# Optimization experiments

Measured on AMD Instinct MI355X. Metric: run time of the kernel, lower is better.

## Reference

```python
import jax, jax.numpy as jnp
import numpy as np

NEG_INF = -1e9  # mask fill value used by the original layer
LEAKY_SLOPE = 0.2


def setup_inputs() -> dict:
    key = jax.random.key(0)
    k1, k2, k3, k4 = jax.random.split(key, 4)
    B, N, D_in = 8, 1024, 256
    H, head_dim = 8, 32  # output_dim=256, concat_heads=True
    node_features = jax.random.normal(k1, (B, N, D_in), dtype=jnp.float32)
    adjacency = jax.random.randint(k2, (B, N, N), 0, 2, dtype=jnp.int32)
    W = jax.random.normal(k3, (H, D_in, head_dim), dtype=jnp.float32) * (1.0 / np.sqrt(D_in))
    a = jax.random.normal(k4, (H, 2 * head_dim), dtype=jnp.float32) * (1.0 / np.sqrt(2 * head_dim))
    bias = jnp.zeros((H * head_dim,), dtype=jnp.float32)
    return {"node_features": node_features, "adjacency": adjacency, "W": W, "a": a, "bias": bias}


def reference(node_features, adjacency, W, a, bias):
    # node_features: (B,N,D_in); adjacency: (B,N,N) in {0,1}
    H, _, hd = W.shape
    # Per-head linear transform: (B,H,N,head_dim)
    Wh = jnp.einsum('bni,hij->bhnj', node_features, W)
    # a @ concat(h_i, h_j) == a1 @ h_i + a2 @ h_j  (avoids O(N^2*2hd) concat)
    a1, a2 = a[:, :hd], a[:, hd:]
    e_i = jnp.einsum('bhnj,hj->bhn', Wh, a1)  # (B,H,N) source term
    e_j = jnp.einsum('bhnj,hj->bhn', Wh, a2)  # (B,H,N) target term
    scores = e_i[:, :, :, None] + e_j[:, :, None, :]  # (B,H,N,N)
    # LeakyReLU(0.2) exactly as ops.maximum(x, 0.2*x)
    scores = jnp.maximum(scores, LEAKY_SLOPE * scores)
    mask = adjacency.astype(scores.dtype)[:, None, :, :]  # (B,1,N,N)
    masked = scores * mask + (1.0 - mask) * NEG_INF
    attn = jax.nn.softmax(masked, axis=-1)  # (B,H,N,N)
    attended = jnp.einsum('bhij,bhjk->bhik', attn, Wh)  # (B,H,N,hd)
    B, _, N, _ = attended.shape
    # concat heads -> (B,N,H*hd); head order matches the python loop concat
    out = attended.transpose(0, 2, 1, 3).reshape(B, N, H * hd)
    out = out + bias
    return jax.nn.relu(out)
```

## Files before the change

kernel.cpp:

```cpp
#include <hip/hip_runtime.h>

#define GAT_B   8
#define GAT_N   1024
#define GAT_DIN 256
#define GAT_H   8
#define GAT_HD  32

typedef unsigned short gu16;
typedef unsigned int   gu32;
typedef __bf16 bf16x8 __attribute__((ext_vector_type(8)));
typedef __bf16 bf16x4 __attribute__((ext_vector_type(4)));
typedef float  f32x4v __attribute__((ext_vector_type(4)));

__device__ __forceinline__ float gb2f(gu16 u) { return __uint_as_float(((gu32)u) << 16); }

__device__ __forceinline__ int gat_is_fp32(const gu16* p) {
    int bad = 0;
    for (int i = 0; i < 128; ++i) {
        int e = (p[i] >> 7) & 0xFF;
        if (e >= 140) bad = 1;
    }
    return bad;
}

__global__ __launch_bounds__(256) void CustomGATLayer_90348932038855_kernel(
    const void* __restrict__ Xv, const void* __restrict__ Wv, const void* __restrict__ Av,
    __bf16* __restrict__ whb, float* __restrict__ e1, float* __restrict__ e2)
{
    __shared__ __align__(16) __bf16 WlF[GAT_DIN * GAT_HD];
    __shared__ int sflag;

    const int t  = threadIdx.x;
    const int id = blockIdx.x;
    const int h  = id & 7;
    const int mg = id >> 3;

    if (t == 0) sflag = gat_is_fp32((const gu16*)Xv);
    __syncthreads();
    const int fp32 = sflag;

    if (fp32) {
        const float* ws = (const float*)Wv + (size_t)h * GAT_DIN * GAT_HD;
        #pragma unroll
        for (int q = 0; q < 8; ++q) {
            int idx = q * 1024 + t * 4;
            int i = idx >> 5, k = idx & 31;
            float4 v = *(const float4*)(ws + idx);
            int d = (((i >> 5) * 4 + ((i >> 3) & 3)) * 32 + k) * 8 + (i & 7);
            WlF[d] = (__bf16)v.x; WlF[d + 8]  = (__bf16)v.y;
            WlF[d + 16] = (__bf16)v.z; WlF[d + 24] = (__bf16)v.w;
        }
    } else {
        const gu16* ws = (const gu16*)Wv + (size_t)h * GAT_DIN * GAT_HD;
        gu16* wl = (gu16*)WlF;
        #pragma unroll
        for (int q = 0; q < 8; ++q) {
            int idx = q * 1024 + t * 4;
            int i = idx >> 5, k = idx & 31;
            ushort4 v = *(const ushort4*)(ws + idx);
            int d = (((i >> 5) * 4 + ((i >> 3) & 3)) * 32 + k) * 8 + (i & 7);
            wl[d] = v.x; wl[d + 8] = v.y; wl[d + 16] = v.z; wl[d + 24] = v.w;
        }
    }
    __syncthreads();

    const int wid = t >> 6, l = t & 63, g = l >> 4, c = l & 15;
    const int mt   = mg * 4 + wid;
    const int M0   = mt * 16;
    const int b    = M0 >> 10;
    const int nloc = M0 & 1023;
    const int row  = nloc + c;

    f32x4v acc0 = {0.f, 0.f, 0.f, 0.f};
    f32x4v acc1 = {0.f, 0.f, 0.f, 0.f};

    if (fp32) {
        const float* xb = (const float*)Xv + ((size_t)b * GAT_N + row) * GAT_DIN;
        #pragma unroll
        for (int kc = 0; kc < 8; ++kc) {
            float4 x0 = *(const float4*)(xb + kc * 32 + 8 * g);
            float4 x1 = *(const float4*)(xb + kc * 32 + 8 * g + 4);
            bf16x8 af;
            af[0] = (__bf16)x0.x; af[1] = (__bf16)x0.y; af[2] = (__bf16)x0.z; af[3] = (__bf16)x0.w;
            af[4] = (__bf16)x1.x; af[5] = (__bf16)x1.y; af[6] = (__bf16)x1.z; af[7] = (__bf16)x1.w;
            bf16x8 b0 = *(const bf16x8*)&WlF[((kc * 4 + g) * 32 + c) * 8];
            bf16x8 b1 = *(const bf16x8*)&WlF[((kc * 4 + g) * 32 + c + 16) * 8];
            acc0 = __builtin_amdgcn_mfma_f32_16x16x32_bf16(af, b0, acc0, 0, 0, 0);
            acc1 = __builtin_amdgcn_mfma_f32_16x16x32_bf16(af, b1, acc1, 0, 0, 0);
        }
    } else {
        const gu16* xb = (const gu16*)Xv + ((size_t)b * GAT_N + row) * GAT_DIN;
        #pragma unroll
        for (int kc = 0; kc < 8; ++kc) {
            bf16x8 af = *(const bf16x8*)(xb + kc * 32 + 8 * g);
            bf16x8 b0 = *(const bf16x8*)&WlF[((kc * 4 + g) * 32 + c) * 8];
            bf16x8 b1 = *(const bf16x8*)&WlF[((kc * 4 + g) * 32 + c + 16) * 8];
            acc0 = __builtin_amdgcn_mfma_f32_16x16x32_bf16(af, b0, acc0, 0, 0, 0);
            acc1 = __builtin_amdgcn_mfma_f32_16x16x32_bf16(af, b1, acc1, 0, 0, 0);
        }
    }

    const int nb = nloc + 4 * g;
    const int jc = nb >> 5, kg = (nb >> 3) & 3, e0 = nb & 7;
    const size_t fb = (((size_t)(b * GAT_H + h) * 32 + jc) * 4 + kg) * 32;
    bf16x4 v0, v1;
    v0[0] = (__bf16)acc0[0]; v0[1] = (__bf16)acc0[1];
    v0[2] = (__bf16)acc0[2]; v0[3] = (__bf16)acc0[3];
    v1[0] = (__bf16)acc1[0]; v1[1] = (__bf16)acc1[1];
    v1[2] = (__bf16)acc1[2]; v1[3] = (__bf16)acc1[3];
    *(bf16x4*)(whb + (fb + c) * 8 + e0)      = v0;
    *(bf16x4*)(whb + (fb + c + 16) * 8 + e0) = v1;

    float a1c, a1c16, a2c, a2c16;
    if (fp32) {
        const float* ap = (const float*)Av + h * 2 * GAT_HD;
        a1c = ap[c]; a1c16 = ap[c + 16]; a2c = ap[32 + c]; a2c16 = ap[48 + c];
    } else {
        const gu16* ap = (const gu16*)Av + h * 2 * GAT_HD;
        a1c = gb2f(ap[c]); a1c16 = gb2f(ap[c + 16]);
        a2c = gb2f(ap[32 + c]); a2c16 = gb2f(ap[48 + c]);
    }
    float p1[4], p2[4];
    #pragma unroll
    for (int q = 0; q < 4; ++q) {
        p1[q] = acc0[q] * a1c + acc1[q] * a1c16;
        p2[q] = acc0[q] * a2c + acc1[q] * a2c16;
        #pragma unroll
        for (int mm = 1; mm <= 8; mm <<= 1) {
            p1[q] += __shfl_xor(p1[q], mm);
            p2[q] += __shfl_xor(p2[q], mm);
        }
    }
    if (c == 0) {
        const size_t eb = (size_t)(b * GAT_H + h) * GAT_N + nb;
        #pragma unroll
        for (int q = 0; q < 4; ++q) { e1[eb + q] = p1[q]; e2[eb + q] = p2[q]; }
    }
}

__global__ __launch_bounds__(512) void CustomGATLayer_90348932038855_attn(
    const void* __restrict__ Xv, const int* __restrict__ adj, const void* __restrict__ biasv,
    const __bf16* __restrict__ whb, const float* __restrict__ e1f, const float* __restrict__ e2f,
    float* __restrict__ out)
{
    __shared__ __align__(16) float e2l[GAT_H * GAT_N];
    __shared__ int sflag;

    const int t = threadIdx.x;
    const int h = t >> 6, l = t & 63, g = l >> 4, c = l & 15;
    const int id = blockIdx.x;
    const int b = id & 7, tile = id >> 3;
    const int i0 = tile * 16;

    if (t == 0) sflag = gat_is_fp32((const gu16*)Xv);

    {
        const float* s = e2f + (size_t)(b * GAT_H + h) * GAT_N;
        float* d = e2l + h * GAT_N;
        #pragma unroll
        for (int q = 0; q < 4; ++q) {
            int off = (q * 64 + l) * 4;
            *(float4*)(d + off) = *(const float4*)(s + off);
        }
    }
    __syncthreads();
    const int fp32 = sflag;

    const float e1r = e1f[(size_t)(b * GAT_H + h) * GAT_N + i0 + c];
    const int* adjr = adj + ((size_t)(b * GAT_N + i0 + c)) * GAT_N + 8 * g;
    const __bf16* whr = whb + (size_t)(b * GAT_H + h) * (GAT_N * GAT_HD) + g * 256 + c * 8;
    const float* e2h = e2l + h * GAT_N + 8 * g;

    int4 pa0 = *(const int4*)(adjr);
    int4 pa1 = *(const int4*)(adjr + 4);
    bf16x8 pw0 = *(const bf16x8*)(whr);
    bf16x8 pw1 = *(const bf16x8*)(whr + 128);

    f32x4v acc0 = {0.f, 0.f, 0.f, 0.f};
    f32x4v acc1 = {0.f, 0.f, 0.f, 0.f};
    float dsum = 0.f;

#define GAT_WCOMP(EV, AV, IDX) {                    \
        float s_ = e1r + (EV);                      \
        s_ = fmaxf(s_, 0.2f * s_);                  \
        s_ = fminf(s_, 60.0f);                      \
        float w_ = __expf(s_);                      \
        w_ = (AV) ? w_ : 0.0f;                      \
        dsum += w_;                                 \
        pf[IDX] = (__bf16)w_; }

    #pragma unroll 4
    for (int jc = 0; jc < 32; ++jc) {
        int4 a0 = pa0, a1 = pa1;
        bf16x8 w0 = pw0, w1 = pw1;
        if (jc < 31) {
            const int* an = adjr + (jc + 1) * 32;
            pa0 = *(const int4*)(an);
            pa1 = *(const int4*)(an + 4);
            const __bf16* wn = whr + (jc + 1) * 1024;
            pw0 = *(const bf16x8*)(wn);
            pw1 = *(const bf16x8*)(wn + 128);
        }
        float4 ea = *(const float4*)(e2h + jc * 32);
        float4 eb = *(const float4*)(e2h + jc * 32 + 4);
        bf16x8 pf;
        GAT_WCOMP(ea.x, a0.x, 0) GAT_WCOMP(ea.y, a0.y, 1)
        GAT_WCOMP(ea.z, a0.z, 2) GAT_WCOMP(ea.w, a0.w, 3)
        GAT_WCOMP(eb.x, a1.x, 4) GAT_WCOMP(eb.y, a1.y, 5)
        GAT_WCOMP(eb.z, a1.z, 6) GAT_WCOMP(eb.w, a1.w, 7)
        acc0 = __builtin_amdgcn_mfma_f32_16x16x32_bf16(pf, w0, acc0, 0, 0, 0);
        acc1 = __builtin_amdgcn_mfma_f32_16x16x32_bf16(pf, w1, acc1, 0, 0, 0);
    }
#undef GAT_WCOMP

    dsum += __shfl_xor(dsum, 16);
    dsum += __shfl_xor(dsum, 32);

    float bv0, bv1;
    if (fp32) {
        const float* bp = (const float*)biasv + h * GAT_HD;
        bv0 = bp[c]; bv1 = bp[c + 16];
    } else {
        const gu16* bp = (const gu16*)biasv + h * GAT_HD;
        bv0 = gb2f(bp[c]); bv1 = gb2f(bp[c + 16]);
    }

    float* ob = out + (size_t)(b * GAT_N + i0) * (GAT_H * GAT_HD) + h * GAT_HD + c;
    #pragma unroll
    for (int q = 0; q < 4; ++q) {
        float d = __shfl(dsum, 4 * g + q);
        float r = (d > 0.f) ? (1.0f / d) : 0.0f;
        float o0 = acc0[q] * r + bv0;
        float o1 = acc1[q] * r + bv1;
        o0 = fmaxf(o0, 0.f); o1 = fmaxf(o1, 0.f);
        ob[(size_t)(4 * g + q) * (GAT_H * GAT_HD)]      = o0;
        ob[(size_t)(4 * g + q) * (GAT_H * GAT_HD) + 16] = o1;
    }
}

extern "C" void kernel_launch(void* const* d_in, const int* in_sizes, int n_in,
                              void* d_out, int out_size, void* d_ws, size_t ws_size,
                              hipStream_t stream) {
    const void* X    = d_in[0];
    const int*  adj  = (const int*)d_in[1];
    const void* Wm   = d_in[2];
    const void* Av   = d_in[3];
    const void* bias = d_in[4];
    float* outp = (float*)d_out;

    __bf16* whb = (__bf16*)d_ws;
    float* e1 = (float*)(whb + (size_t)GAT_B * GAT_H * GAT_N * GAT_HD);
    float* e2 = e1 + (size_t)GAT_B * GAT_H * GAT_N;

    CustomGATLayer_90348932038855_kernel
        <<<dim3(128 * GAT_H), 256, 0, stream>>>(X, Wm, Av, whb, e1, e2);
    CustomGATLayer_90348932038855_attn
        <<<dim3((GAT_N / 16) * GAT_B), 512, 0, stream>>>(
            X, adj, bias, whb, e1, e2, outp);
}
```

Baseline: 136.1 us.

## Retile projection kernel, deepen attention prefetch, use exp2 and MFMA row sums

The projection kernel now runs 256 blocks of 512 threads, each handling two row tiles per wave. W fragments are hoisted into registers under a reordered LDS layout, and format detection uses a wave ballot instead of a serial loop. The attention kernel prefetches adjacency three chunks ahead and Wh two ahead. It folds log2e into the attention vector so it can use exp2, and computes the softmax denominator with an extra MFMA against a ones vector instead of scalar sums and shuffles. The aim is less latency and fewer ALU and shuffle operations, at the cost of higher register pressure and bf16 rounding in the denominator.

```diff
diff --git a/kernel.cpp b/kernel.cpp
--- a/kernel.cpp
+++ b/kernel.cpp
@@ -5,6 +5,7 @@
 #define GAT_DIN 256
 #define GAT_H   8
 #define GAT_HD  32
+#define GAT_LOG2E 1.4426950408889634f
 
 typedef unsigned short gu16;
 typedef unsigned int   gu32;
@@ -12,18 +13,24 @@
 typedef __bf16 bf16x4 __attribute__((ext_vector_type(4)));
 typedef float  f32x4v __attribute__((ext_vector_type(4)));
 
+#if __has_builtin(__builtin_amdgcn_exp2f)
+#define GAT_EXP2(x) __builtin_amdgcn_exp2f(x)
+#else
+#define GAT_EXP2(x) exp2f(x)
+#endif
+
 __device__ __forceinline__ float gb2f(gu16 u) { return __uint_as_float(((gu32)u) << 16); }
 
-__device__ __forceinline__ int gat_is_fp32(const gu16* p) {
-    int bad = 0;
-    for (int i = 0; i < 128; ++i) {
-        int e = (p[i] >> 7) & 0xFF;
-        if (e >= 140) bad = 1;
-    }
-    return bad;
-}
-
-__global__ __launch_bounds__(256) void CustomGATLayer_90348932038855_kernel(
+__device__ __forceinline__ void gat_detect(const gu16* p, int t, int* sflag) {
+    if (t < 64) {
+        int e0 = (p[2 * t]     >> 7) & 0xFF;
+        int e1 = (p[2 * t + 1] >> 7) & 0xFF;
+        unsigned long long m = __ballot((e0 >= 140) || (e1 >= 140));
+        if (t == 0) *sflag = (m != 0ULL);
+    }
+}
+
+__global__ __launch_bounds__(512) void CustomGATLayer_90348932038855_kernel(
     const void* __restrict__ Xv, const void* __restrict__ Wv, const void* __restrict__ Av,
     __bf16* __restrict__ whb, float* __restrict__ e1, float* __restrict__ e2)
 {
@@ -32,109 +39,118 @@
 
     const int t  = threadIdx.x;
     const int id = blockIdx.x;
-    const int h  = id & 7;
-    const int mg = id >> 3;
-
-    if (t == 0) sflag = gat_is_fp32((const gu16*)Xv);
+    const int h  = id >> 5;
+    const int mg = id & 31;
+
+    gat_detect((const gu16*)Xv, t, &sflag);
     __syncthreads();
     const int fp32 = sflag;
 
     if (fp32) {
         const float* ws = (const float*)Wv + (size_t)h * GAT_DIN * GAT_HD;
         #pragma unroll
-        for (int q = 0; q < 8; ++q) {
-            int idx = q * 1024 + t * 4;
+        for (int q = 0; q < 4; ++q) {
+            int idx = q * 2048 + t * 4;
             int i = idx >> 5, k = idx & 31;
             float4 v = *(const float4*)(ws + idx);
-            int d = (((i >> 5) * 4 + ((i >> 3) & 3)) * 32 + k) * 8 + (i & 7);
-            WlF[d] = (__bf16)v.x; WlF[d + 8]  = (__bf16)v.y;
-            WlF[d + 16] = (__bf16)v.z; WlF[d + 24] = (__bf16)v.w;
+            int d = (((i >> 5) * 32 + k) * 4 + ((i >> 3) & 3)) * 8 + (i & 7);
+            WlF[d] = (__bf16)v.x; WlF[d + 32] = (__bf16)v.y;
+            WlF[d + 64] = (__bf16)v.z; WlF[d + 96] = (__bf16)v.w;
         }
     } else {
         const gu16* ws = (const gu16*)Wv + (size_t)h * GAT_DIN * GAT_HD;
         gu16* wl = (gu16*)WlF;
         #pragma unroll
-        for (int q = 0; q < 8; ++q) {
-            int idx = q * 1024 + t * 4;
+        for (int q = 0; q < 4; ++q) {
+            int idx = q * 2048 + t * 4;
             int i = idx >> 5, k = idx & 31;
             ushort4 v = *(const ushort4*)(ws + idx);
-            int d = (((i >> 5) * 4 + ((i >> 3) & 3)) * 32 + k) * 8 + (i & 7);
-            wl[d] = v.x; wl[d + 8] = v.y; wl[d + 16] = v.z; wl[d + 24] = v.w;
+            int d = (((i >> 5) * 32 + k) * 4 + ((i >> 3) & 3)) * 8 + (i & 7);
+            wl[d] = v.x; wl[d + 32] = v.y; wl[d + 64] = v.z; wl[d + 96] = v.w;
         }
     }
     __syncthreads();
 
     const int wid = t >> 6, l = t & 63, g = l >> 4, c = l & 15;
-    const int mt   = mg * 4 + wid;
-    const int M0   = mt * 16;
-    const int b    = M0 >> 10;
-    const int nloc = M0 & 1023;
-    const int row  = nloc + c;
-
-    f32x4v acc0 = {0.f, 0.f, 0.f, 0.f};
-    f32x4v acc1 = {0.f, 0.f, 0.f, 0.f};
-
-    if (fp32) {
-        const float* xb = (const float*)Xv + ((size_t)b * GAT_N + row) * GAT_DIN;
-        #pragma unroll
-        for (int kc = 0; kc < 8; ++kc) {
-            float4 x0 = *(const float4*)(xb + kc * 32 + 8 * g);
-            float4 x1 = *(const float4*)(xb + kc * 32 + 8 * g + 4);
-            bf16x8 af;
-            af[0] = (__bf16)x0.x; af[1] = (__bf16)x0.y; af[2] = (__bf16)x0.z; af[3] = (__bf16)x0.w;
-            af[4] = (__bf16)x1.x; af[5] = (__bf16)x1.y; af[6] = (__bf16)x1.z; af[7] = (__bf16)x1.w;
-            bf16x8 b0 = *(const bf16x8*)&WlF[((kc * 4 + g) * 32 + c) * 8];
-            bf16x8 b1 = *(const bf16x8*)&WlF[((kc * 4 + g) * 32 + c + 16) * 8];
-            acc0 = __builtin_amdgcn_mfma_f32_16x16x32_bf16(af, b0, acc0, 0, 0, 0);
-            acc1 = __builtin_amdgcn_mfma_f32_16x16x32_bf16(af, b1, acc1, 0, 0, 0);
-        }
-    } else {
-        const gu16* xb = (const gu16*)Xv + ((size_t)b * GAT_N + row) * GAT_DIN;
-        #pragma unroll
-        for (int kc = 0; kc < 8; ++kc) {
-            bf16x8 af = *(const bf16x8*)(xb + kc * 32 + 8 * g);
-            bf16x8 b0 = *(const bf16x8*)&WlF[((kc * 4 + g) * 32 + c) * 8];
-            bf16x8 b1 = *(const bf16x8*)&WlF[((kc * 4 + g) * 32 + c + 16) * 8];
-            acc0 = __builtin_amdgcn_mfma_f32_16x16x32_bf16(af, b0, acc0, 0, 0, 0);
-            acc1 = __builtin_amdgcn_mfma_f32_16x16x32_bf16(af, b1, acc1, 0, 0, 0);
-        }
-    }
-
-    const int nb = nloc + 4 * g;
-    const int jc = nb >> 5, kg = (nb >> 3) & 3, e0 = nb & 7;
-    const size_t fb = (((size_t)(b * GAT_H + h) * 32 + jc) * 4 + kg) * 32;
-    bf16x4 v0, v1;
-    v0[0] = (__bf16)acc0[0]; v0[1] = (__bf16)acc0[1];
-    v0[2] = (__bf16)acc0[2]; v0[3] = (__bf16)acc0[3];
-    v1[0] = (__bf16)acc1[0]; v1[1] = (__bf16)acc1[1];
-    v1[2] = (__bf16)acc1[2]; v1[3] = (__bf16)acc1[3];
-    *(bf16x4*)(whb + (fb + c) * 8 + e0)      = v0;
-    *(bf16x4*)(whb + (fb + c + 16) * 8 + e0) = v1;
+
+    bf16x8 bf0[8], bf1[8];
+    #pragma unroll
+    for (int kc = 0; kc < 8; ++kc) {
+        bf0[kc] = *(const bf16x8*)&WlF[((kc * 32 + c) * 4 + g) * 8];
+        bf1[kc] = *(const bf16x8*)&WlF[((kc * 32 + c + 16) * 4 + g) * 8];
+    }
 
     float a1c, a1c16, a2c, a2c16;
     if (fp32) {
         const float* ap = (const float*)Av + h * 2 * GAT_HD;
-        a1c = ap[c]; a1c16 = ap[c + 16]; a2c = ap[32 + c]; a2c16 = ap[48 + c];
+        a1c = ap[c] * GAT_LOG2E;      a1c16 = ap[c + 16] * GAT_LOG2E;
+        a2c = ap[32 + c] * GAT_LOG2E; a2c16 = ap[48 + c] * GAT_LOG2E;
     } else {
         const gu16* ap = (const gu16*)Av + h * 2 * GAT_HD;
-        a1c = gb2f(ap[c]); a1c16 = gb2f(ap[c + 16]);
-        a2c = gb2f(ap[32 + c]); a2c16 = gb2f(ap[48 + c]);
-    }
-    float p1[4], p2[4];
-    #pragma unroll
-    for (int q = 0; q < 4; ++q) {
-        p1[q] = acc0[q] * a1c + acc1[q] * a1c16;
-        p2[q] = acc0[q] * a2c + acc1[q] * a2c16;
-        #pragma unroll
-        for (int mm = 1; mm <= 8; mm <<= 1) {
-            p1[q] += __shfl_xor(p1[q], mm);
-            p2[q] += __shfl_xor(p2[q], mm);
-        }
-    }
-    if (c == 0) {
-        const size_t eb = (size_t)(b * GAT_H + h) * GAT_N + nb;
-        #pragma unroll
-        for (int q = 0; q < 4; ++q) { e1[eb + q] = p1[q]; e2[eb + q] = p2[q]; }
+        a1c = gb2f(ap[c]) * GAT_LOG2E;      a1c16 = gb2f(ap[c + 16]) * GAT_LOG2E;
+        a2c = gb2f(ap[32 + c]) * GAT_LOG2E; a2c16 = gb2f(ap[48 + c]) * GAT_LOG2E;
+    }
+
+    #pragma unroll
+    for (int tt = 0; tt < 2; ++tt) {
+        const int mt   = mg * 16 + wid * 2 + tt;
+        const int M0   = mt * 16;
+        const int b    = M0 >> 10;
+        const int nloc = M0 & 1023;
+        const int row  = nloc + c;
+
+        f32x4v acc0 = {0.f, 0.f, 0.f, 0.f};
+        f32x4v acc1 = {0.f, 0.f, 0.f, 0.f};
+
+        if (fp32) {
+            const float* xb = (const float*)Xv + ((size_t)b * GAT_N + row) * GAT_DIN;
+            #pragma unroll
+            for (int kc = 0; kc < 8; ++kc) {
+                float4 x0 = *(const float4*)(xb + kc * 32 + 8 * g);
+                float4 x1 = *(const float4*)(xb + kc * 32 + 8 * g + 4);
+                bf16x8 af;
+                af[0] = (__bf16)x0.x; af[1] = (__bf16)x0.y; af[2] = (__bf16)x0.z; af[3] = (__bf16)x0.w;
+                af[4] = (__bf16)x1.x; af[5] = (__bf16)x1.y; af[6] = (__bf16)x1.z; af[7] = (__bf16)x1.w;
+                acc0 = __builtin_amdgcn_mfma_f32_16x16x32_bf16(af, bf0[kc], acc0, 0, 0, 0);
+                acc1 = __builtin_amdgcn_mfma_f32_16x16x32_bf16(af, bf1[kc], acc1, 0, 0, 0);
+            }
+        } else {
+            const gu16* xb = (const gu16*)Xv + ((size_t)b * GAT_N + row) * GAT_DIN;
+            #pragma unroll
+            for (int kc = 0; kc < 8; ++kc) {
+                bf16x8 af = *(const bf16x8*)(xb + kc * 32 + 8 * g);
+                acc0 = __builtin_amdgcn_mfma_f32_16x16x32_bf16(af, bf0[kc], acc0, 0, 0, 0);
+                acc1 = __builtin_amdgcn_mfma_f32_16x16x32_bf16(af, bf1[kc], acc1, 0, 0, 0);
+            }
+        }
+
+        const int nb = nloc + 4 * g;
+        const int jcc = nb >> 5, kg = (nb >> 3) & 3, e0 = nb & 7;
+        const size_t fb = (((size_t)(b * GAT_H + h) * 32 + jcc) * 4 + kg) * 32;
+        bf16x4 v0, v1;
+        v0[0] = (__bf16)acc0[0]; v0[1] = (__bf16)acc0[1];
+        v0[2] = (__bf16)acc0[2]; v0[3] = (__bf16)acc0[3];
+        v1[0] = (__bf16)acc1[0]; v1[1] = (__bf16)acc1[1];
+        v1[2] = (__bf16)acc1[2]; v1[3] = (__bf16)acc1[3];
+        *(bf16x4*)(whb + (fb + c) * 8 + e0)      = v0;
+        *(bf16x4*)(whb + (fb + c + 16) * 8 + e0) = v1;
+
+        float p1[4], p2[4];
+        #pragma unroll
+        for (int q = 0; q < 4; ++q) {
+            p1[q] = acc0[q] * a1c + acc1[q] * a1c16;
+            p2[q] = acc0[q] * a2c + acc1[q] * a2c16;
+            #pragma unroll
+            for (int mm = 1; mm <= 8; mm <<= 1) {
+                p1[q] += __shfl_xor(p1[q], mm);
+                p2[q] += __shfl_xor(p2[q], mm);
+            }
+        }
+        if (c == 0) {
+            const size_t eb = (size_t)(b * GAT_H + h) * GAT_N + nb;
+            #pragma unroll
+            for (int q = 0; q < 4; ++q) { e1[eb + q] = p1[q]; e2[eb + q] = p2[q]; }
+        }
     }
 }
 
@@ -152,7 +168,7 @@
     const int b = id & 7, tile = id >> 3;
     const int i0 = tile * 16;
 
-    if (t == 0) sflag = gat_is_fp32((const gu16*)Xv);
+    gat_detect((const gu16*)Xv, t, &sflag);
 
     {
         const float* s = e2f + (size_t)(b * GAT_H + h) * GAT_N;
@@ -171,35 +187,40 @@
     const __bf16* whr = whb + (size_t)(b * GAT_H + h) * (GAT_N * GAT_HD) + g * 256 + c * 8;
     const float* e2h = e2l + h * GAT_N + 8 * g;
 
-    int4 pa0 = *(const int4*)(adjr);
-    int4 pa1 = *(const int4*)(adjr + 4);
-    bf16x8 pw0 = *(const bf16x8*)(whr);
-    bf16x8 pw1 = *(const bf16x8*)(whr + 128);
+    int4 aA0 = *(const int4*)(adjr),      aA1 = *(const int4*)(adjr + 4);
+    int4 aB0 = *(const int4*)(adjr + 32), aB1 = *(const int4*)(adjr + 36);
+    int4 aC0 = *(const int4*)(adjr + 64), aC1 = *(const int4*)(adjr + 68);
+    bf16x8 wA0 = *(const bf16x8*)(whr),        wA1 = *(const bf16x8*)(whr + 128);
+    bf16x8 wB0 = *(const bf16x8*)(whr + 1024), wB1 = *(const bf16x8*)(whr + 1152);
 
     f32x4v acc0 = {0.f, 0.f, 0.f, 0.f};
     f32x4v acc1 = {0.f, 0.f, 0.f, 0.f};
-    float dsum = 0.f;
+    f32x4v accS = {0.f, 0.f, 0.f, 0.f};
+    bf16x8 onesf;
+    #pragma unroll
+    for (int e = 0; e < 8; ++e) onesf[e] = (__bf16)1.0f;
 
 #define GAT_WCOMP(EV, AV, IDX) {                    \
         float s_ = e1r + (EV);                      \
         s_ = fmaxf(s_, 0.2f * s_);                  \
-        s_ = fminf(s_, 60.0f);                      \
-        float w_ = __expf(s_);                      \
+        s_ = fminf(s_, 86.0f);                      \
+        float w_ = GAT_EXP2(s_);                    \
         w_ = (AV) ? w_ : 0.0f;                      \
-        dsum += w_;                                 \
         pf[IDX] = (__bf16)w_; }
 
-    #pragma unroll 4
+    #pragma unroll 2
     for (int jc = 0; jc < 32; ++jc) {
-        int4 a0 = pa0, a1 = pa1;
-        bf16x8 w0 = pw0, w1 = pw1;
-        if (jc < 31) {
-            const int* an = adjr + (jc + 1) * 32;
-            pa0 = *(const int4*)(an);
-            pa1 = *(const int4*)(an + 4);
-            const __bf16* wn = whr + (jc + 1) * 1024;
-            pw0 = *(const bf16x8*)(wn);
-            pw1 = *(const bf16x8*)(wn + 128);
+        const int4 a0 = aA0, a1 = aA1;
+        const bf16x8 w0 = wA0, w1 = wA1;
+        aA0 = aB0; aA1 = aB1; aB0 = aC0; aB1 = aC1;
+        wA0 = wB0; wA1 = wB1;
+        if (jc < 29) {
+            const int* an = adjr + (jc + 3) * 32;
+            aC0 = *(const int4*)an; aC1 = *(const int4*)(an + 4);
+        }
+        if (jc < 30) {
+            const __bf16* wn = whr + (jc + 2) * 1024;
+            wB0 = *(const bf16x8*)wn; wB1 = *(const bf16x8*)(wn + 128);
         }
         float4 ea = *(const float4*)(e2h + jc * 32);
         float4 eb = *(const float4*)(e2h + jc * 32 + 4);
@@ -210,11 +231,9 @@
         GAT_WCOMP(eb.z, a1.z, 6) GAT_WCOMP(eb.w, a1.w, 7)
         acc0 = __builtin_amdgcn_mfma_f32_16x16x32_bf16(pf, w0, acc0, 0, 0, 0);
         acc1 = __builtin_amdgcn_mfma_f32_16x16x32_bf16(pf, w1, acc1, 0, 0, 0);
+        accS = __builtin_amdgcn_mfma_f32_16x16x32_bf16(pf, onesf, accS, 0, 0, 0);
     }
 #undef GAT_WCOMP
-
-    dsum += __shfl_xor(dsum, 16);
-    dsum += __shfl_xor(dsum, 32);
 
     float bv0, bv1;
     if (fp32) {
@@ -228,11 +247,10 @@
     float* ob = out + (size_t)(b * GAT_N + i0) * (GAT_H * GAT_HD) + h * GAT_HD + c;
     #pragma unroll
     for (int q = 0; q < 4; ++q) {
-        float d = __shfl(dsum, 4 * g + q);
+        float d = accS[q];
         float r = (d > 0.f) ? (1.0f / d) : 0.0f;
-        float o0 = acc0[q] * r + bv0;
-        float o1 = acc1[q] * r + bv1;
-        o0 = fmaxf(o0, 0.f); o1 = fmaxf(o1, 0.f);
+        float o0 = fmaxf(acc0[q] * r + bv0, 0.f);
+        float o1 = fmaxf(acc1[q] * r + bv1, 0.f);
         ob[(size_t)(4 * g + q) * (GAT_H * GAT_HD)]      = o0;
         ob[(size_t)(4 * g + q) * (GAT_H * GAT_HD) + 16] = o1;
     }
@@ -253,7 +271,7 @@
     float* e2 = e1 + (size_t)GAT_B * GAT_H * GAT_N;
 
     CustomGATLayer_90348932038855_kernel
-        <<<dim3(128 * GAT_H), 256, 0, stream>>>(X, Wm, Av, whb, e1, e2);
+        <<<dim3(8 * 32), 512, 0, stream>>>(X, Wm, Av, whb, e1, e2);
     CustomGATLayer_90348932038855_attn
         <<<dim3((GAT_N / 16) * GAT_B), 512, 0, stream>>>(
             X, adj, bias, whb, e1, e2, outp);
```

Measured after the change: 134.3 us. Within noise of the previous version (-1.3%).
